# Performance work log

Measured on AMD Instinct MI355X. Metric: run time of the kernel, lower is better.

Reference implementation:

```python
import jax, jax.numpy as jnp
import numpy as np

EPS = 1e-6

def setup_inputs() -> dict:
    key = jax.random.key(0)
    ks = jax.random.split(key, 9)
    B, D, F = 8192, 2048, 1024
    s_in = 1.0 / np.sqrt(D)
    return {
        "Q": jax.random.normal(ks[0], (B, D), jnp.float32),
        "K": jax.random.normal(ks[1], (B, D), jnp.float32),
        "V": jax.random.normal(ks[2], (B, D), jnp.float32),
        "Wq": jax.random.normal(ks[3], (D, F), jnp.float32) * s_in,
        "bq": jnp.zeros((F,), jnp.float32),
        "Wk": jax.random.normal(ks[4], (D, F), jnp.float32) * s_in,
        "bk": jnp.zeros((F,), jnp.float32),
        "Wv": jax.random.normal(ks[5], (D, D), jnp.float32) * s_in,
        "bv": jnp.zeros((D,), jnp.float32),
    }

def reference(Q, K, V, Wq, bq, Wk, bk, Wv, bv):
    # feature maps: Linear + ELU (note: ELU, no +1, matching the source)
    Q_feat = jax.nn.elu(Q @ Wq + bq)          # (B, F)
    K_feat = jax.nn.elu(K @ Wk + bk)          # (B, F)
    V_proj = V @ Wv + bv                      # (B, D)
    # torch: KV = outer(K_feat, V_proj); QKV = Q_feat @ KV
    # equivalent without materializing (B, F, D):
    qk = jnp.einsum('bi,bi->b', Q_feat, K_feat)      # (B,)
    QKV = qk[:, None] * V_proj                        # (B, D)
    # Z = 1 / (sum_i Q_feat * sum_i K_feat + eps)
    Z = 1.0 / (Q_feat.sum(-1) * K_feat.sum(-1) + EPS)  # (B,)
    return QKV * Z[:, None]
```

## Files before the change

### kernel.cpp

```cpp
#include <hip/hip_runtime.h>
#include <hip/hip_fp16.h>
#include <cstdint>
#include <cstddef>

typedef _Float16 f16x8 __attribute__((ext_vector_type(8)));
typedef _Float16 f16x4 __attribute__((ext_vector_type(4)));
typedef float    f32x4 __attribute__((ext_vector_type(4)));

#define GPTR(p) ((const __attribute__((address_space(1))) void*)(p))
#define SPTR(p) ((__attribute__((address_space(3))) void*)(p))

__global__ void transpose_cast_kernel(const float* __restrict__ W,
                                      _Float16* __restrict__ Wt,
                                      int R, int C) {
  __shared__ float tile[32][33];
  const int c  = blockIdx.x * 32 + threadIdx.x;
  const int r0 = blockIdx.y * 32;
  for (int i = threadIdx.y; i < 32; i += 8)
    tile[i][threadIdx.x] = W[(size_t)(r0 + i) * C + c];
  __syncthreads();
  const int out_c = r0 + threadIdx.x;
  const int oc0   = blockIdx.x * 32;
  for (int i = threadIdx.y; i < 32; i += 8)
    Wt[(size_t)(oc0 + i) * R + out_c] = (_Float16)tile[threadIdx.x][i];
}

__global__ void cast_f32_f16_kernel(const float* __restrict__ src,
                                    _Float16* __restrict__ dst) {
  const size_t i = (size_t)blockIdx.x * 256 + threadIdx.x;
  const float4 v = ((const float4*)src)[i];
  f16x4 h;
  h[0] = (_Float16)v.x; h[1] = (_Float16)v.y;
  h[2] = (_Float16)v.z; h[3] = (_Float16)v.w;
  ((f16x4*)dst)[i] = h;
}

template <int MODE, bool AHALF, bool OUTHALF>
__global__ __launch_bounds__(256) void gemm2(
    const void* __restrict__ Av,
    const _Float16* __restrict__ Bt0, const _Float16* __restrict__ Bt1,
    const float* __restrict__ bias0, const float* __restrict__ bias1,
    int msplit, const float* __restrict__ scale,
    void* __restrict__ Cv, int K, int N) {
  constexpr int BK = 64;
  __shared__ __align__(16) _Float16 As[128 * BK];
  __shared__ __align__(16) _Float16 Bs[128 * BK];

  const int tid  = threadIdx.x;
  const int lane = tid & 63;
  const int wave = tid >> 6;
  const int quad = lane >> 4;
  const int r    = lane & 15;
  const int wm   = wave >> 1;
  const int wn   = wave & 1;
  const int m0   = blockIdx.y * 128;
  const int n0   = blockIdx.x * 128;

  const _Float16* Bt  = (m0 >= msplit) ? Bt1 : Bt0;
  const float* bias   = (m0 >= msplit) ? bias1 : bias0;

  size_t aoff[4], boff[4];
  int slot[4];
#pragma unroll
  for (int t = 0; t < 4; ++t) {
    const int s  = wave * 256 + t * 64 + lane;
    const int n  = s >> 3;
    const int kc = (s & 7) ^ (n & 7);
    aoff[t] = (size_t)(m0 + n) * K + kc * 8;
    boff[t] = (size_t)(n0 + n) * K + kc * 8;
    slot[t] = s;
  }

  f32x4 acc[4][4] = {};
  const _Float16* Ah = (const _Float16*)Av;
  const float*    Af = (const float*)Av;

  for (int k0 = 0; k0 < K; k0 += BK) {
    __syncthreads();
    if (AHALF) {
#pragma unroll
      for (int t = 0; t < 4; ++t)
        __builtin_amdgcn_global_load_lds(GPTR(Ah + aoff[t] + k0),
                                         SPTR(As + (wave * 256 + t * 64) * 8),
                                         16, 0, 0);
    } else {
#pragma unroll
      for (int t = 0; t < 4; ++t) {
        const float* ap = Af + aoff[t] + k0;
        const float4 v0 = *(const float4*)ap;
        const float4 v1 = *(const float4*)(ap + 4);
        f16x8 h;
        h[0] = (_Float16)v0.x; h[1] = (_Float16)v0.y;
        h[2] = (_Float16)v0.z; h[3] = (_Float16)v0.w;
        h[4] = (_Float16)v1.x; h[5] = (_Float16)v1.y;
        h[6] = (_Float16)v1.z; h[7] = (_Float16)v1.w;
        *(f16x8*)(As + (size_t)slot[t] * 8) = h;
      }
    }
#pragma unroll
    for (int t = 0; t < 4; ++t)
      __builtin_amdgcn_global_load_lds(GPTR(Bt + boff[t] + k0),
                                       SPTR(Bs + (wave * 256 + t * 64) * 8),
                                       16, 0, 0);
    __syncthreads();

#pragma unroll
    for (int ki = 0; ki < 2; ++ki) {
      f16x8 af[4], bf[4];
#pragma unroll
      for (int i = 0; i < 4; ++i) {
        const int an = wm * 64 + i * 16 + r;
        af[i] = *(const f16x8*)(As + (an * 8 + ((ki * 4 + quad) ^ (an & 7))) * 8);
      }
#pragma unroll
      for (int j = 0; j < 4; ++j) {
        const int bn = wn * 64 + j * 16 + r;
        bf[j] = *(const f16x8*)(Bs + (bn * 8 + ((ki * 4 + quad) ^ (bn & 7))) * 8);
      }
#pragma unroll
      for (int i = 0; i < 4; ++i)
#pragma unroll
        for (int j = 0; j < 4; ++j)
          acc[i][j] = __builtin_amdgcn_mfma_f32_16x16x32_f16(af[i], bf[j],
                                                             acc[i][j], 0, 0, 0);
    }
  }

  float*    Cf = (float*)Cv;
  _Float16* Ch = (_Float16*)Cv;
#pragma unroll
  for (int i = 0; i < 4; ++i) {
#pragma unroll
    for (int j = 0; j < 4; ++j) {
      const int col = n0 + wn * 64 + j * 16 + r;
      const float b = bias[col];
#pragma unroll
      for (int reg = 0; reg < 4; ++reg) {
        const int row = m0 + wm * 64 + i * 16 + quad * 4 + reg;
        float v = acc[i][j][reg] + b;
        if (MODE == 0) v = v > 0.f ? v : (expf(v) - 1.f);
        else           v = v * scale[row];
        if (OUTHALF) Ch[(size_t)row * N + col] = (_Float16)v;
        else         Cf[(size_t)row * N + col] = v;
      }
    }
  }
}

template <bool HALF>
__global__ void reduce_scale2(const void* __restrict__ Qf,
                              const void* __restrict__ Kf,
                              float* __restrict__ scale) {
  const int b = blockIdx.x;
  const int t = threadIdx.x;
  float q[4], k[4];
  if (HALF) {
    const f16x4 qh = ((const f16x4*)((const _Float16*)Qf + (size_t)b * 1024))[t];
    const f16x4 kh = ((const f16x4*)((const _Float16*)Kf + (size_t)b * 1024))[t];
#pragma unroll
    for (int i = 0; i < 4; ++i) { q[i] = (float)qh[i]; k[i] = (float)kh[i]; }
  } else {
    const float4 qv = ((const float4*)((const float*)Qf + (size_t)b * 1024))[t];
    const float4 kv = ((const float4*)((const float*)Kf + (size_t)b * 1024))[t];
    q[0] = qv.x; q[1] = qv.y; q[2] = qv.z; q[3] = qv.w;
    k[0] = kv.x; k[1] = kv.y; k[2] = kv.z; k[3] = kv.w;
  }
  float qk = q[0] * k[0] + q[1] * k[1] + q[2] * k[2] + q[3] * k[3];
  float sq = q[0] + q[1] + q[2] + q[3];
  float sk = k[0] + k[1] + k[2] + k[3];
#pragma unroll
  for (int off = 32; off > 0; off >>= 1) {
    qk += __shfl_down(qk, off, 64);
    sq += __shfl_down(sq, off, 64);
    sk += __shfl_down(sk, off, 64);
  }
  __shared__ float buf[3][4];
  const int lane = t & 63, wv = t >> 6;
  if (lane == 0) { buf[0][wv] = qk; buf[1][wv] = sq; buf[2][wv] = sk; }
  __syncthreads();
  if (t == 0) {
    const float QK = buf[0][0] + buf[0][1] + buf[0][2] + buf[0][3];
    const float SQ = buf[1][0] + buf[1][1] + buf[1][2] + buf[1][3];
    const float SK = buf[2][0] + buf[2][1] + buf[2][2] + buf[2][3];
    scale[b] = QK / (SQ * SK + 1e-6f);
  }
}

extern "C" void kernel_launch(void* const* d_in, const int* in_sizes, int n_in,
                              void* d_out, int out_size, void* d_ws,
                              size_t ws_size, hipStream_t stream) {
  const float* Q  = (const float*)d_in[0];
  const float* K_ = (const float*)d_in[1];
  const float* V  = (const float*)d_in[2];
  const float* Wq = (const float*)d_in[3];
  const float* bq = (const float*)d_in[4];
  const float* Wk = (const float*)d_in[5];
  const float* bk = (const float*)d_in[6];
  const float* Wv = (const float*)d_in[7];
  const float* bv = (const float*)d_in[8];
  float* out = (float*)d_out;

  const int B = 8192, D = 2048, F = 1024;
  const size_t MiB = 1u << 20;
  char* ws = (char*)d_ws;

  const size_t NEED_FAST = 40 * MiB + 64 * 1024;

  if (ws_size >= NEED_FAST) {
    _Float16* WqT = (_Float16*)ws;
    _Float16* WkT = (_Float16*)(ws + 4 * MiB);
    _Float16* WvT = (_Float16*)ws;
    _Float16* QfH = (_Float16*)(ws + 8 * MiB);
    _Float16* KfH = (_Float16*)(ws + 24 * MiB);
    _Float16* Vh  = (_Float16*)(ws + 8 * MiB);
    float* scale  = (float*)(ws + 40 * MiB);
    _Float16* Qh = (_Float16*)d_out;
    _Float16* Kh = (_Float16*)d_out + (size_t)B * D;

    dim3 tb(32, 8);
    transpose_cast_kernel<<<dim3(F / 32, D / 32), tb, 0, stream>>>(Wq, WqT, D, F);
    transpose_cast_kernel<<<dim3(F / 32, D / 32), tb, 0, stream>>>(Wk, WkT, D, F);
    const int castBlocks = (B * D / 4) / 256;
    cast_f32_f16_kernel<<<castBlocks, 256, 0, stream>>>(Q,  Qh);
    cast_f32_f16_kernel<<<castBlocks, 256, 0, stream>>>(K_, Kh);

    gemm2<0, true, true><<<dim3(F / 128, (2 * B) / 128), 256, 0, stream>>>(
        Qh, WqT, WkT, bq, bk, B, nullptr, QfH, D, F);
    reduce_scale2<true><<<B, 256, 0, stream>>>(QfH, KfH, scale);

    cast_f32_f16_kernel<<<castBlocks, 256, 0, stream>>>(V, Vh);
    transpose_cast_kernel<<<dim3(D / 32, D / 32), tb, 0, stream>>>(Wv, WvT, D, D);
    gemm2<1, true, false><<<dim3(D / 128, B / 128), 256, 0, stream>>>(
        Vh, WvT, WvT, bv, bv, 1 << 30, scale, out, D, D);
  } else {
    _Float16* WqT = (_Float16*)ws;
    _Float16* WkT = (_Float16*)(ws + 4 * MiB);
    _Float16* WvT = (_Float16*)(ws + 8 * MiB);
    float* scale  = (float*)(ws + 16 * MiB);
    float* Qf = out;
    float* Kf = out + (size_t)B * F;

    dim3 tb(32, 8);
    transpose_cast_kernel<<<dim3(F / 32, D / 32), tb, 0, stream>>>(Wq, WqT, D, F);
    transpose_cast_kernel<<<dim3(F / 32, D / 32), tb, 0, stream>>>(Wk, WkT, D, F);
    transpose_cast_kernel<<<dim3(D / 32, D / 32), tb, 0, stream>>>(Wv, WvT, D, D);

    gemm2<0, false, false><<<dim3(F / 128, B / 128), 256, 0, stream>>>(
        Q, WqT, WqT, bq, bq, 1 << 30, nullptr, Qf, D, F);
    gemm2<0, false, false><<<dim3(F / 128, B / 128), 256, 0, stream>>>(
        K_, WkT, WkT, bk, bk, 1 << 30, nullptr, Kf, D, F);
    reduce_scale2<false><<<B, 256, 0, stream>>>(Qf, Kf, scale);
    gemm2<1, false, false><<<dim3(D / 128, B / 128), 256, 0, stream>>>(
        V, WvT, WvT, bv, bv, 1 << 30, scale, out, D, D);
  }
}
```

Baseline: 440.8 us.

## Switch GEMM to 32x32x16 MFMA and batch cast/transpose launches

Replaces the 16x16x32 MFMA tiling with 32x32x16 MFMA, so each wave issues fewer, larger matrix instructions and loads fewer LDS fragments per k-step. It also merges the separate weight transpose-cast and activation cast kernels into multi-tensor kernels, cutting launch count. A new workspace path keeps all converted tensors in separate buffers so every conversion runs up front. The epilogue row mapping changes to the 32x32 accumulator layout, which adds some risk of indexing errors and of higher register pressure.

Result: slower. 481.8 us (+9.3%).

```diff
diff --git a/kernel.cpp b/kernel.cpp
--- a/kernel.cpp
+++ b/kernel.cpp
@@ -3,16 +3,27 @@
 #include <cstdint>
 #include <cstddef>
 
-typedef _Float16 f16x8 __attribute__((ext_vector_type(8)));
-typedef _Float16 f16x4 __attribute__((ext_vector_type(4)));
-typedef float    f32x4 __attribute__((ext_vector_type(4)));
+typedef _Float16 f16x8  __attribute__((ext_vector_type(8)));
+typedef _Float16 f16x4  __attribute__((ext_vector_type(4)));
+typedef float    f32x4  __attribute__((ext_vector_type(4)));
+typedef float    f32x16 __attribute__((ext_vector_type(16)));
 
 #define GPTR(p) ((const __attribute__((address_space(1))) void*)(p))
 #define SPTR(p) ((__attribute__((address_space(3))) void*)(p))
 
-__global__ void transpose_cast_kernel(const float* __restrict__ W,
-                                      _Float16* __restrict__ Wt,
-                                      int R, int C) {
+__global__ void transpose_cast3(const float* __restrict__ W0,
+                                const float* __restrict__ W1,
+                                const float* __restrict__ W2,
+                                _Float16* __restrict__ T0,
+                                _Float16* __restrict__ T1,
+                                _Float16* __restrict__ T2,
+                                int R, int C0, int C1, int C2) {
+  const int z = blockIdx.z;
+  const float* W = (z == 0) ? W0 : (z == 1) ? W1 : W2;
+  _Float16*    T = (z == 0) ? T0 : (z == 1) ? T1 : T2;
+  const int    C = (z == 0) ? C0 : (z == 1) ? C1 : C2;
+  if (blockIdx.x * 32 >= C) return;
+
   __shared__ float tile[32][33];
   const int c  = blockIdx.x * 32 + threadIdx.x;
   const int r0 = blockIdx.y * 32;
@@ -22,12 +33,19 @@
   const int out_c = r0 + threadIdx.x;
   const int oc0   = blockIdx.x * 32;
   for (int i = threadIdx.y; i < 32; i += 8)
-    Wt[(size_t)(oc0 + i) * R + out_c] = (_Float16)tile[threadIdx.x][i];
-}
-
-__global__ void cast_f32_f16_kernel(const float* __restrict__ src,
-                                    _Float16* __restrict__ dst) {
-  const size_t i = (size_t)blockIdx.x * 256 + threadIdx.x;
+    T[(size_t)(oc0 + i) * R + out_c] = (_Float16)tile[threadIdx.x][i];
+}
+
+__global__ void cast3_f32_f16(const float* __restrict__ S0,
+                              const float* __restrict__ S1,
+                              const float* __restrict__ S2,
+                              _Float16* __restrict__ D0,
+                              _Float16* __restrict__ D1,
+                              _Float16* __restrict__ D2) {
+  const int idx = blockIdx.x >> 14;
+  const float* src = (idx == 0) ? S0 : (idx == 1) ? S1 : S2;
+  _Float16*    dst = (idx == 0) ? D0 : (idx == 1) ? D1 : D2;
+  const size_t i = (size_t)(blockIdx.x & 16383) * 256 + threadIdx.x;
   const float4 v = ((const float4*)src)[i];
   f16x4 h;
   h[0] = (_Float16)v.x; h[1] = (_Float16)v.y;
@@ -49,15 +67,15 @@
   const int tid  = threadIdx.x;
   const int lane = tid & 63;
   const int wave = tid >> 6;
-  const int quad = lane >> 4;
-  const int r    = lane & 15;
+  const int l31  = lane & 31;
+  const int khalf = lane >> 5;
   const int wm   = wave >> 1;
   const int wn   = wave & 1;
   const int m0   = blockIdx.y * 128;
   const int n0   = blockIdx.x * 128;
 
-  const _Float16* Bt  = (m0 >= msplit) ? Bt1 : Bt0;
-  const float* bias   = (m0 >= msplit) ? bias1 : bias0;
+  const _Float16* Bt = (m0 >= msplit) ? Bt1 : Bt0;
+  const float* bias  = (m0 >= msplit) ? bias1 : bias0;
 
   size_t aoff[4], boff[4];
   int slot[4];
@@ -71,7 +89,7 @@
     slot[t] = s;
   }
 
-  f32x4 acc[4][4] = {};
+  f32x16 acc[2][2] = {};
   const _Float16* Ah = (const _Float16*)Av;
   const float*    Af = (const float*)Av;
 
@@ -105,39 +123,38 @@
     __syncthreads();
 
 #pragma unroll
-    for (int ki = 0; ki < 2; ++ki) {
-      f16x8 af[4], bf[4];
-#pragma unroll
-      for (int i = 0; i < 4; ++i) {
-        const int an = wm * 64 + i * 16 + r;
-        af[i] = *(const f16x8*)(As + (an * 8 + ((ki * 4 + quad) ^ (an & 7))) * 8);
+    for (int c = 0; c < 4; ++c) {
+      const int kc = c * 2 + khalf;
+      f16x8 af[2], bf[2];
+#pragma unroll
+      for (int t = 0; t < 2; ++t) {
+        const int an = wm * 64 + t * 32 + l31;
+        af[t] = *(const f16x8*)(As + (an * 8 + (kc ^ (an & 7))) * 8);
+        const int bn = wn * 64 + t * 32 + l31;
+        bf[t] = *(const f16x8*)(Bs + (bn * 8 + (kc ^ (bn & 7))) * 8);
       }
 #pragma unroll
-      for (int j = 0; j < 4; ++j) {
-        const int bn = wn * 64 + j * 16 + r;
-        bf[j] = *(const f16x8*)(Bs + (bn * 8 + ((ki * 4 + quad) ^ (bn & 7))) * 8);
-      }
-#pragma unroll
-      for (int i = 0; i < 4; ++i)
-#pragma unroll
-        for (int j = 0; j < 4; ++j)
-          acc[i][j] = __builtin_amdgcn_mfma_f32_16x16x32_f16(af[i], bf[j],
-                                                             acc[i][j], 0, 0, 0);
+      for (int ti = 0; ti < 2; ++ti)
+#pragma unroll
+        for (int tj = 0; tj < 2; ++tj)
+          acc[ti][tj] = __builtin_amdgcn_mfma_f32_32x32x16_f16(
+              af[ti], bf[tj], acc[ti][tj], 0, 0, 0);
     }
   }
 
   float*    Cf = (float*)Cv;
   _Float16* Ch = (_Float16*)Cv;
 #pragma unroll
-  for (int i = 0; i < 4; ++i) {
-#pragma unroll
-    for (int j = 0; j < 4; ++j) {
-      const int col = n0 + wn * 64 + j * 16 + r;
+  for (int ti = 0; ti < 2; ++ti) {
+#pragma unroll
+    for (int tj = 0; tj < 2; ++tj) {
+      const int col = n0 + wn * 64 + tj * 32 + l31;
       const float b = bias[col];
 #pragma unroll
-      for (int reg = 0; reg < 4; ++reg) {
-        const int row = m0 + wm * 64 + i * 16 + quad * 4 + reg;
-        float v = acc[i][j][reg] + b;
+      for (int reg = 0; reg < 16; ++reg) {
+        const int row =
+            m0 + wm * 64 + ti * 32 + (reg & 3) + 8 * (reg >> 2) + 4 * khalf;
+        float v = acc[ti][tj][reg] + b;
         if (MODE == 0) v = v > 0.f ? v : (expf(v) - 1.f);
         else           v = v * scale[row];
         if (OUTHALF) Ch[(size_t)row * N + col] = (_Float16)v;
@@ -204,9 +221,30 @@
   const size_t MiB = 1u << 20;
   char* ws = (char*)d_ws;
 
+  const size_t NEED_BIG  = 80 * MiB + 64 * 1024;
   const size_t NEED_FAST = 40 * MiB + 64 * 1024;
 
-  if (ws_size >= NEED_FAST) {
+  if (ws_size >= NEED_BIG) {
+    _Float16* WqT = (_Float16*)ws;
+    _Float16* WkT = (_Float16*)(ws + 4 * MiB);
+    _Float16* WvT = (_Float16*)(ws + 8 * MiB);
+    _Float16* QfH = (_Float16*)(ws + 16 * MiB);
+    _Float16* KfH = (_Float16*)(ws + 32 * MiB);
+    _Float16* Vh  = (_Float16*)(ws + 48 * MiB);
+    float* scale  = (float*)(ws + 80 * MiB);
+    _Float16* Qh = (_Float16*)d_out;
+    _Float16* Kh = (_Float16*)d_out + (size_t)B * D;
+
+    transpose_cast3<<<dim3(64, 64, 3), dim3(32, 8), 0, stream>>>(
+        Wq, Wk, Wv, WqT, WkT, WvT, D, F, F, D);
+    cast3_f32_f16<<<3 * 16384, 256, 0, stream>>>(Q, K_, V, Qh, Kh, Vh);
+
+    gemm2<0, true, true><<<dim3(F / 128, (2 * B) / 128), 256, 0, stream>>>(
+        Qh, WqT, WkT, bq, bk, B, nullptr, QfH, D, F);
+    reduce_scale2<true><<<B, 256, 0, stream>>>(QfH, KfH, scale);
+    gemm2<1, true, false><<<dim3(D / 128, B / 128), 256, 0, stream>>>(
+        Vh, WvT, WvT, bv, bv, 1 << 30, scale, out, D, D);
+  } else if (ws_size >= NEED_FAST) {
     _Float16* WqT = (_Float16*)ws;
     _Float16* WkT = (_Float16*)(ws + 4 * MiB);
     _Float16* WvT = (_Float16*)ws;
@@ -217,19 +255,17 @@
     _Float16* Qh = (_Float16*)d_out;
     _Float16* Kh = (_Float16*)d_out + (size_t)B * D;
 
-    dim3 tb(32, 8);
-    transpose_cast_kernel<<<dim3(F / 32, D / 32), tb, 0, stream>>>(Wq, WqT, D, F);
-    transpose_cast_kernel<<<dim3(F / 32, D / 32), tb, 0, stream>>>(Wk, WkT, D, F);
-    const int castBlocks = (B * D / 4) / 256;
-    cast_f32_f16_kernel<<<castBlocks, 256, 0, stream>>>(Q,  Qh);
-    cast_f32_f16_kernel<<<castBlocks, 256, 0, stream>>>(K_, Kh);
+    transpose_cast3<<<dim3(32, 64, 2), dim3(32, 8), 0, stream>>>(
+        Wq, Wk, Wk, WqT, WkT, WkT, D, F, F, F);
+    cast3_f32_f16<<<2 * 16384, 256, 0, stream>>>(Q, K_, K_, Qh, Kh, Kh);
 
     gemm2<0, true, true><<<dim3(F / 128, (2 * B) / 128), 256, 0, stream>>>(
         Qh, WqT, WkT, bq, bk, B, nullptr, QfH, D, F);
     reduce_scale2<true><<<B, 256, 0, stream>>>(QfH, KfH, scale);
 
-    cast_f32_f16_kernel<<<castBlocks, 256, 0, stream>>>(V, Vh);
-    transpose_cast_kernel<<<dim3(D / 32, D / 32), tb, 0, stream>>>(Wv, WvT, D, D);
+    cast3_f32_f16<<<16384, 256, 0, stream>>>(V, V, V, Vh, Vh, Vh);
+    transpose_cast3<<<dim3(64, 64, 1), dim3(32, 8), 0, stream>>>(
+        Wv, Wv, Wv, WvT, WvT, WvT, D, D, D, D);
     gemm2<1, true, false><<<dim3(D / 128, B / 128), 256, 0, stream>>>(
         Vh, WvT, WvT, bv, bv, 1 << 30, scale, out, D, D);
   } else {
@@ -240,11 +276,8 @@
     float* Qf = out;
     float* Kf = out + (size_t)B * F;
 
-    dim3 tb(32, 8);
-    transpose_cast_kernel<<<dim3(F / 32, D / 32), tb, 0, stream>>>(Wq, WqT, D, F);
-    transpose_cast_kernel<<<dim3(F / 32, D / 32), tb, 0, stream>>>(Wk, WkT, D, F);
-    transpose_cast_kernel<<<dim3(D / 32, D / 32), tb, 0, stream>>>(Wv, WvT, D, D);
-
+    transpose_cast3<<<dim3(64, 64, 3), dim3(32, 8), 0, stream>>>(
+        Wq, Wk, Wv, WqT, WkT, WvT, D, F, F, D);
     gemm2<0, false, false><<<dim3(F / 128, B / 128), 256, 0, stream>>>(
         Q, WqT, WqT, bq, bq, 1 << 30, nullptr, Qf, D, F);
     gemm2<0, false, false><<<dim3(F / 128, B / 128), 256, 0, stream>>>(
```
